# Performance work log

Hardware: AMD Instinct MI355X
Metric: run time of the kernel (lower is better)

The kernel has to match this reference:

```python
import jax, jax.numpy as jnp
import numpy as np

N_NODES = 140000   # 14 frames * 10000 nodes/frame
N_EDGES = 2240000  # avg degree 16
NFEAT = 128
NHID = 128
N_FRAMES = 14


def setup_inputs() -> dict:
    key = jax.random.key(0)
    k1, k2, k3, k4, k5 = jax.random.split(key, 5)
    x = jax.random.normal(k1, (N_NODES, NFEAT), dtype=jnp.float32)
    # gc1 parameters (only layer actually used in forward)
    W = jax.random.normal(k2, (NFEAT, NHID), dtype=jnp.float32) * 0.05
    b = jnp.zeros((NHID,), dtype=jnp.float32)
    # sparse normalized adjacency as COO edge list (row sorted for fast segment_sum)
    edge_row = jnp.sort(jax.random.randint(k3, (N_EDGES,), 0, N_NODES, dtype=jnp.int32))
    edge_col = jax.random.randint(k4, (N_EDGES,), 0, N_NODES, dtype=jnp.int32)
    edge_val = jax.random.uniform(k5, (N_EDGES,), dtype=jnp.float32)
    return {"x": x, "W": W, "b": b, "edge_val": edge_val,
            "edge_row": edge_row, "edge_col": edge_col}


def reference(x, W, b, edge_val, edge_row, edge_col):
    # GraphConvolution: adj @ (x @ W) + b  (adj sparse, COO)
    support = x @ W                                   # [N, NHID]
    msgs = edge_val[:, None] * support[edge_col]      # [E, NHID] gather
    agg = jax.ops.segment_sum(msgs, edge_row, num_segments=N_NODES,
                              indices_are_sorted=True)  # [N, NHID] scatter-add
    h = jax.nn.relu(agg + b)
    # view(14, -1, c) then max over frame axis
    h = h.reshape(N_FRAMES, -1, NHID)                 # [14, N/14, NHID]
    h = jnp.max(h, axis=0)                            # [N/14, NHID]
    return jax.nn.log_softmax(h, axis=1)
```

## Files before the change

kernel.cpp:

```cpp
#include <hip/hip_runtime.h>
#include <hip/hip_bf16.h>

#define N_NODES 140000
#define N_EDGES 2240000
#define NFEAT 128
#define NHID 128
#define N_FRAMES 14
#define NODES_PER_FRAME 10000
#define CAP 352

typedef __attribute__((ext_vector_type(8))) short frag_b16;
typedef __attribute__((ext_vector_type(4))) int frag_i4;
typedef __attribute__((ext_vector_type(4))) float f32x4;

__device__ __forceinline__ unsigned short f2bf(float f) {
    union { float f; unsigned int u; } v; v.f = f;
    unsigned int r = v.u + 0x7fffu + ((v.u >> 16) & 1u);
    return (unsigned short)(r >> 16);
}
__device__ __forceinline__ int pk_bf16(float a, float b) {
    union { __hip_bfloat162 h; int i; } u;
    u.h = __float22bfloat162_rn(make_float2(a, b));
    return u.i;
}

__global__ void convert_wt(const float* __restrict__ W, unsigned short* __restrict__ WT) {
    int idx = blockIdx.x * blockDim.x + threadIdx.x;
    if (idx >= NFEAT * NHID) return;
    int k = idx >> 7, n = idx & 127;
    WT[n * 128 + k] = f2bf(W[idx]);
}

#define WT_STRIDE 136

__global__ __launch_bounds__(256) void gemm_kernel(
        const float* __restrict__ x, const unsigned short* __restrict__ WT,
        unsigned char* __restrict__ supQ, float* __restrict__ scales) {
    __shared__ unsigned short wt_lds[128 * WT_STRIDE];

    const uint4* WTv = (const uint4*)WT;
    for (int idx = threadIdx.x; idx < 2048; idx += 256) {
        uint4 d = WTv[idx];
        int elem = idx << 3;
        int n = elem >> 7, k = elem & 127;
        *(uint4*)&wt_lds[n * WT_STRIDE + k] = d;
    }

    int wave = threadIdx.x >> 6;
    int lane = threadIdx.x & 63;
    int m = lane & 15;
    int q = lane >> 4;

    long row0 = (long)blockIdx.x * 64 + wave * 16;

    int arow = (int)row0 + m;
    if (arow >= N_NODES) arow = N_NODES - 1;
    const float* xrow = x + (long)arow * 128 + q * 8;
    frag_b16 xa[4];
#pragma unroll
    for (int ks = 0; ks < 4; ++ks) {
        float4 lo = *(const float4*)(xrow + ks * 32);
        float4 hi = *(const float4*)(xrow + ks * 32 + 4);
        union { frag_b16 f; frag_i4 i; } u;
        u.i[0] = pk_bf16(lo.x, lo.y);
        u.i[1] = pk_bf16(lo.z, lo.w);
        u.i[2] = pk_bf16(hi.x, hi.y);
        u.i[3] = pk_bf16(hi.z, hi.w);
        xa[ks] = u.f;
    }

    __syncthreads();

    if (row0 < N_NODES) {
        f32x4 acc[8];
#pragma unroll
        for (int t = 0; t < 8; ++t) acc[t] = (f32x4){0.f, 0.f, 0.f, 0.f};

#pragma unroll
        for (int t = 0; t < 8; ++t) {
            const unsigned short* bp = &wt_lds[(t * 16 + m) * WT_STRIDE + q * 8];
#pragma unroll
            for (int ks = 0; ks < 4; ++ks) {
                frag_b16 wfrag = *(const frag_b16*)(bp + ks * 32);
                acc[t] = __builtin_amdgcn_mfma_f32_16x16x32_bf16(wfrag, xa[ks], acc[t], 0, 0, 0);
            }
        }

        float amax = 0.f;
#pragma unroll
        for (int t = 0; t < 8; ++t)
#pragma unroll
            for (int r = 0; r < 4; ++r) amax = fmaxf(amax, fabsf(acc[t][r]));
        amax = fmaxf(amax, __shfl_xor(amax, 16));
        amax = fmaxf(amax, __shfl_xor(amax, 32));
        float rinv = amax > 0.f ? 127.f / amax : 0.f;

        long node = row0 + m;
        if (node < N_NODES) {
            if (q == 0) scales[node] = amax * (1.f / 127.f);
            unsigned char* srow = supQ + node * 128;
#pragma unroll
            for (int t = 0; t < 8; ++t) {
                unsigned u0 = (unsigned)(rintf(acc[t][0] * rinv) + 128.f);
                unsigned u1 = (unsigned)(rintf(acc[t][1] * rinv) + 128.f);
                unsigned u2 = (unsigned)(rintf(acc[t][2] * rinv) + 128.f);
                unsigned u3 = (unsigned)(rintf(acc[t][3] * rinv) + 128.f);
                *(unsigned*)(srow + t * 16 + q * 4) = u0 | (u1 << 8) | (u2 << 16) | (u3 << 24);
            }
        }
    }
}

__global__ void prep_kernel(const int* __restrict__ edge_row, const int* __restrict__ edge_col,
                            const float* __restrict__ edge_val, const float* __restrict__ scales,
                            int* __restrict__ row_ptr, float* __restrict__ valp) {
    int e = blockIdx.x * blockDim.x + threadIdx.x;
    if (e >= N_EDGES) return;
    int r = edge_row[e];
    int prev = (e == 0) ? -1 : edge_row[e - 1];
    for (int q = prev + 1; q <= r; ++q) row_ptr[q] = e;
    if (e == N_EDGES - 1) {
        for (int q = r + 1; q <= N_NODES; ++q) row_ptr[q] = N_EDGES;
    }
    valp[e] = edge_val[e] * scales[edge_col[e]];
}

__global__ __launch_bounds__(128) void agg_kernel(
        const unsigned char* __restrict__ supQ, const float* __restrict__ b,
        const float* __restrict__ valp, const int* __restrict__ edge_col,
        const int* __restrict__ row_ptr, float* __restrict__ out) {
    __shared__ int    segStart[2][8];
    __shared__ int    segLen[2][8];
    __shared__ int    segOff[2][8];
    __shared__ int2   eBuf[2][CAP];
    __shared__ float4 xch[2][16][2];

    const int i = blockIdx.x;
    const int lane = threadIdx.x & 63;
    const int w = threadIdx.x >> 6;
    const int eh = lane >> 4;
    const int f8 = lane & 15;
    const unsigned f8x8 = (unsigned)f8 * 8u;

    int a = 0, len = 0;
    if (lane < 7) {
        int n = (w * 7 + lane) * NODES_PER_FRAME + i;
        a = row_ptr[n];
        len = row_ptr[n + 1] - a;
    }
    int len8 = (len + 7) & ~7;
    int off = 0;
#pragma unroll
    for (int f2 = 0; f2 < 7; ++f2) {
        int L2 = __shfl(len8, f2);
        if (f2 < lane) off += L2;
    }
    if (lane < 7) { segStart[w][lane] = a; segLen[w][lane] = len; segOff[w][lane] = off; }
    if (lane == 6) segOff[w][7] = off + len8;
    __syncthreads();

    const bool fit = segOff[w][7] <= CAP;

    if (fit) {
#pragma unroll 1
        for (int f = 0; f < 7; ++f) {
            int g = segStart[w][f], s = segOff[w][f], L = segLen[w][f];
            int L8 = (L + 7) & ~7;
            for (int j = lane; j < L8; j += 64) {
                int2 v = make_int2(0, 0);
                if (j < L) {
                    v.x = edge_col[g + j];
                    v.y = __float_as_int(valp[g + j]);
                }
                eBuf[w][s + j] = v;
            }
        }
    }
    __syncthreads();

    const float4 blo = *(const float4*)&b[f8 * 8];
    const float4 bhi = *(const float4*)&b[f8 * 8 + 4];
    float m0 = 0.f, m1 = 0.f, m2 = 0.f, m3 = 0.f;
    float m4 = 0.f, m5 = 0.f, m6 = 0.f, m7 = 0.f;

    if (fit) {
#pragma unroll 1
        for (int f = 0; f < 7; ++f) {
            int s = segOff[w][f];
            int e8 = s + ((segLen[w][f] + 7) & ~7);
            float a0 = 0.f, a1 = 0.f, a2 = 0.f, a3 = 0.f;
            float a4 = 0.f, a5 = 0.f, a6 = 0.f, a7 = 0.f, svf = 0.f;
            for (int j = s; j < e8; j += 8) {
                int2 e0 = eBuf[w][j + eh];
                int2 e1 = eBuf[w][j + 4 + eh];
                uint2 q0 = *(const uint2*)(supQ + (((unsigned)e0.x) << 7) + f8x8);
                uint2 q1 = *(const uint2*)(supQ + (((unsigned)e1.x) << 7) + f8x8);
                float v0 = __int_as_float(e0.y);
                float v1 = __int_as_float(e1.y);
                a0 = fmaf(v0, (float)( q0.x        & 0xffu), a0);
                a1 = fmaf(v0, (float)((q0.x >> 8)  & 0xffu), a1);
                a2 = fmaf(v0, (float)((q0.x >> 16) & 0xffu), a2);
                a3 = fmaf(v0, (float)( q0.x >> 24        ), a3);
                a4 = fmaf(v0, (float)( q0.y        & 0xffu), a4);
                a5 = fmaf(v0, (float)((q0.y >> 8)  & 0xffu), a5);
                a6 = fmaf(v0, (float)((q0.y >> 16) & 0xffu), a6);
                a7 = fmaf(v0, (float)( q0.y >> 24        ), a7);
                svf += v0;
                a0 = fmaf(v1, (float)( q1.x        & 0xffu), a0);
                a1 = fmaf(v1, (float)((q1.x >> 8)  & 0xffu), a1);
                a2 = fmaf(v1, (float)((q1.x >> 16) & 0xffu), a2);
                a3 = fmaf(v1, (float)( q1.x >> 24        ), a3);
                a4 = fmaf(v1, (float)( q1.y        & 0xffu), a4);
                a5 = fmaf(v1, (float)((q1.y >> 8)  & 0xffu), a5);
                a6 = fmaf(v1, (float)((q1.y >> 16) & 0xffu), a6);
                a7 = fmaf(v1, (float)( q1.y >> 24        ), a7);
                svf += v1;
            }
            a0 += __shfl_xor(a0, 16); a1 += __shfl_xor(a1, 16);
            a2 += __shfl_xor(a2, 16); a3 += __shfl_xor(a3, 16);
            a4 += __shfl_xor(a4, 16); a5 += __shfl_xor(a5, 16);
            a6 += __shfl_xor(a6, 16); a7 += __shfl_xor(a7, 16);
            svf += __shfl_xor(svf, 16);
            a0 += __shfl_xor(a0, 32); a1 += __shfl_xor(a1, 32);
            a2 += __shfl_xor(a2, 32); a3 += __shfl_xor(a3, 32);
            a4 += __shfl_xor(a4, 32); a5 += __shfl_xor(a5, 32);
            a6 += __shfl_xor(a6, 32); a7 += __shfl_xor(a7, 32);
            svf += __shfl_xor(svf, 32);
            float h0 = fmaf(-128.f, svf, a0) + blo.x;
            float h1 = fmaf(-128.f, svf, a1) + blo.y;
            float h2 = fmaf(-128.f, svf, a2) + blo.z;
            float h3 = fmaf(-128.f, svf, a3) + blo.w;
            float h4 = fmaf(-128.f, svf, a4) + bhi.x;
            float h5 = fmaf(-128.f, svf, a5) + bhi.y;
            float h6 = fmaf(-128.f, svf, a6) + bhi.z;
            float h7 = fmaf(-128.f, svf, a7) + bhi.w;
            m0 = fmaxf(m0, fmaxf(h0, 0.f)); m1 = fmaxf(m1, fmaxf(h1, 0.f));
            m2 = fmaxf(m2, fmaxf(h2, 0.f)); m3 = fmaxf(m3, fmaxf(h3, 0.f));
            m4 = fmaxf(m4, fmaxf(h4, 0.f)); m5 = fmaxf(m5, fmaxf(h5, 0.f));
            m6 = fmaxf(m6, fmaxf(h6, 0.f)); m7 = fmaxf(m7, fmaxf(h7, 0.f));
        }
    } else {
#pragma unroll 1
        for (int f = 0; f < 7; ++f) {
            int g = segStart[w][f], L = segLen[w][f];
            float a0 = 0.f, a1 = 0.f, a2 = 0.f, a3 = 0.f;
            float a4 = 0.f, a5 = 0.f, a6 = 0.f, a7 = 0.f, svf = 0.f;
            for (int j = eh; j < L; j += 4) {
                int c = edge_col[g + j];
                float v = valp[g + j];
                uint2 qv = *(const uint2*)(supQ + (((unsigned)c) << 7) + f8x8);
                a0 = fmaf(v, (float)( qv.x        & 0xffu), a0);
                a1 = fmaf(v, (float)((qv.x >> 8)  & 0xffu), a1);
                a2 = fmaf(v, (float)((qv.x >> 16) & 0xffu), a2);
                a3 = fmaf(v, (float)( qv.x >> 24        ), a3);
                a4 = fmaf(v, (float)( qv.y        & 0xffu), a4);
                a5 = fmaf(v, (float)((qv.y >> 8)  & 0xffu), a5);
                a6 = fmaf(v, (float)((qv.y >> 16) & 0xffu), a6);
                a7 = fmaf(v, (float)( qv.y >> 24        ), a7);
                svf += v;
            }
            a0 += __shfl_xor(a0, 16); a1 += __shfl_xor(a1, 16);
            a2 += __shfl_xor(a2, 16); a3 += __shfl_xor(a3, 16);
            a4 += __shfl_xor(a4, 16); a5 += __shfl_xor(a5, 16);
            a6 += __shfl_xor(a6, 16); a7 += __shfl_xor(a7, 16);
            svf += __shfl_xor(svf, 16);
            a0 += __shfl_xor(a0, 32); a1 += __shfl_xor(a1, 32);
            a2 += __shfl_xor(a2, 32); a3 += __shfl_xor(a3, 32);
            a4 += __shfl_xor(a4, 32); a5 += __shfl_xor(a5, 32);
            a6 += __shfl_xor(a6, 32); a7 += __shfl_xor(a7, 32);
            svf += __shfl_xor(svf, 32);
            float h0 = fmaf(-128.f, svf, a0) + blo.x;
            float h1 = fmaf(-128.f, svf, a1) + blo.y;
            float h2 = fmaf(-128.f, svf, a2) + blo.z;
            float h3 = fmaf(-128.f, svf, a3) + blo.w;
            float h4 = fmaf(-128.f, svf, a4) + bhi.x;
            float h5 = fmaf(-128.f, svf, a5) + bhi.y;
            float h6 = fmaf(-128.f, svf, a6) + bhi.z;
            float h7 = fmaf(-128.f, svf, a7) + bhi.w;
            m0 = fmaxf(m0, fmaxf(h0, 0.f)); m1 = fmaxf(m1, fmaxf(h1, 0.f));
            m2 = fmaxf(m2, fmaxf(h2, 0.f)); m3 = fmaxf(m3, fmaxf(h3, 0.f));
            m4 = fmaxf(m4, fmaxf(h4, 0.f)); m5 = fmaxf(m5, fmaxf(h5, 0.f));
            m6 = fmaxf(m6, fmaxf(h6, 0.f)); m7 = fmaxf(m7, fmaxf(h7, 0.f));
        }
    }

    if (eh == 0) {
        xch[w][f8][0] = make_float4(m0, m1, m2, m3);
        xch[w][f8][1] = make_float4(m4, m5, m6, m7);
    }
    __syncthreads();
    float4 p0 = xch[0][f8][0], p1 = xch[0][f8][1];
    float4 q0 = xch[1][f8][0], q1 = xch[1][f8][1];
    float o0 = fmaxf(p0.x, q0.x), o1 = fmaxf(p0.y, q0.y);
    float o2 = fmaxf(p0.z, q0.z), o3 = fmaxf(p0.w, q0.w);
    float o4 = fmaxf(p1.x, q1.x), o5 = fmaxf(p1.y, q1.y);
    float o6 = fmaxf(p1.z, q1.z), o7 = fmaxf(p1.w, q1.w);

    float M = fmaxf(fmaxf(fmaxf(o0, o1), fmaxf(o2, o3)),
                    fmaxf(fmaxf(o4, o5), fmaxf(o6, o7)));
#pragma unroll
    for (int o = 8; o >= 1; o >>= 1) M = fmaxf(M, __shfl_xor(M, o));
    float S = __expf(o0 - M) + __expf(o1 - M) + __expf(o2 - M) + __expf(o3 - M)
            + __expf(o4 - M) + __expf(o5 - M) + __expf(o6 - M) + __expf(o7 - M);
#pragma unroll
    for (int o = 8; o >= 1; o >>= 1) S += __shfl_xor(S, o);

    if (w == 0 && eh == 0) {
        float ls = __logf(S);
        float* orow = out + i * 128 + f8 * 8;
        *(float4*)orow       = make_float4(o0 - M - ls, o1 - M - ls, o2 - M - ls, o3 - M - ls);
        *(float4*)(orow + 4) = make_float4(o4 - M - ls, o5 - M - ls, o6 - M - ls, o7 - M - ls);
    }
}

extern "C" void kernel_launch(void* const* d_in, const int* in_sizes, int n_in,
                              void* d_out, int out_size, void* d_ws, size_t ws_size,
                              hipStream_t stream) {
    const float* x        = (const float*)d_in[0];
    const float* W        = (const float*)d_in[1];
    const float* b        = (const float*)d_in[2];
    const float* edge_val = (const float*)d_in[3];
    const int*   edge_row = (const int*)d_in[4];
    const int*   edge_col = (const int*)d_in[5];
    float* out = (float*)d_out;

    char* ws = (char*)d_ws;
    unsigned char*  supQ    = (unsigned char*)ws;
    float*          scales  = (float*)(ws + 17920000);
    unsigned short* WT      = (unsigned short*)(ws + 18480000);
    int*            row_ptr = (int*)(ws + 18512768);
    float*          valp    = (float*)(ws + 19072772);

    convert_wt<<<64, 256, 0, stream>>>(W, WT);
    gemm_kernel<<<(N_NODES + 63) / 64, 256, 0, stream>>>(x, WT, supQ, scales);
    prep_kernel<<<(N_EDGES + 255) / 256, 256, 0, stream>>>(edge_row, edge_col, edge_val,
                                                           scales, row_ptr, valp);
    agg_kernel<<<NODES_PER_FRAME, 128, 0, stream>>>(supQ, b, valp, edge_col, row_ptr, out);
}
```

Before: 213.0 us.

## Fold edge scaling into aggregation, merge prep kernels, software-pipeline gathers

The weight-transpose conversion is merged with the row_ptr construction into a single prep kernel launched before the GEMM. The valp array (edge_val times the per-column scale) is no longer materialized; the aggregation kernel computes it while staging edges into LDS, and stores the column pre-shifted as a byte offset. This removes one launch and a full write and read of the per-edge array, at the cost of an extra random scales gather inside the aggregation kernel. The fast-path gather loop is also software-pipelined, loading the next pair of rows while the current pair is accumulated, to hide gather latency at some extra register cost.

Result: faster. 207.9 us (-2.4%).

```diff
diff --git a/kernel.cpp b/kernel.cpp
--- a/kernel.cpp
+++ b/kernel.cpp
@@ -24,11 +24,21 @@
     return u.i;
 }
 
-__global__ void convert_wt(const float* __restrict__ W, unsigned short* __restrict__ WT) {
-    int idx = blockIdx.x * blockDim.x + threadIdx.x;
-    if (idx >= NFEAT * NHID) return;
-    int k = idx >> 7, n = idx & 127;
-    WT[n * 128 + k] = f2bf(W[idx]);
+__global__ void prep_kernel(const float* __restrict__ W, unsigned short* __restrict__ WT,
+                            const int* __restrict__ edge_row, int* __restrict__ row_ptr) {
+    int e = blockIdx.x * blockDim.x + threadIdx.x;
+    if (e < NFEAT * NHID) {
+        int k = e >> 7, n = e & 127;
+        WT[n * 128 + k] = f2bf(W[e]);
+    }
+    if (e < N_EDGES) {
+        int r = edge_row[e];
+        int prev = (e == 0) ? -1 : edge_row[e - 1];
+        for (int q = prev + 1; q <= r; ++q) row_ptr[q] = e;
+        if (e == N_EDGES - 1) {
+            for (int q = r + 1; q <= N_NODES; ++q) row_ptr[q] = N_EDGES;
+        }
+    }
 }
 
 #define WT_STRIDE 136
@@ -111,23 +121,10 @@
     }
 }
 
-__global__ void prep_kernel(const int* __restrict__ edge_row, const int* __restrict__ edge_col,
-                            const float* __restrict__ edge_val, const float* __restrict__ scales,
-                            int* __restrict__ row_ptr, float* __restrict__ valp) {
-    int e = blockIdx.x * blockDim.x + threadIdx.x;
-    if (e >= N_EDGES) return;
-    int r = edge_row[e];
-    int prev = (e == 0) ? -1 : edge_row[e - 1];
-    for (int q = prev + 1; q <= r; ++q) row_ptr[q] = e;
-    if (e == N_EDGES - 1) {
-        for (int q = r + 1; q <= N_NODES; ++q) row_ptr[q] = N_EDGES;
-    }
-    valp[e] = edge_val[e] * scales[edge_col[e]];
-}
-
 __global__ __launch_bounds__(128) void agg_kernel(
-        const unsigned char* __restrict__ supQ, const float* __restrict__ b,
-        const float* __restrict__ valp, const int* __restrict__ edge_col,
+        const unsigned char* __restrict__ supQ, const float* __restrict__ scales,
+        const float* __restrict__ b,
+        const float* __restrict__ edge_val, const int* __restrict__ edge_col,
         const int* __restrict__ row_ptr, float* __restrict__ out) {
     __shared__ int    segStart[2][8];
     __shared__ int    segLen[2][8];
@@ -169,8 +166,9 @@
             for (int j = lane; j < L8; j += 64) {
                 int2 v = make_int2(0, 0);
                 if (j < L) {
-                    v.x = edge_col[g + j];
-                    v.y = __float_as_int(valp[g + j]);
+                    int c = edge_col[g + j];
+                    v.x = c << 7;
+                    v.y = __float_as_int(edge_val[g + j] * scales[c]);
                 }
                 eBuf[w][s + j] = v;
             }
@@ -187,35 +185,69 @@
 #pragma unroll 1
         for (int f = 0; f < 7; ++f) {
             int s = segOff[w][f];
-            int e8 = s + ((segLen[w][f] + 7) & ~7);
+            int R = ((segLen[w][f] + 7) & ~7) >> 3;
             float a0 = 0.f, a1 = 0.f, a2 = 0.f, a3 = 0.f;
             float a4 = 0.f, a5 = 0.f, a6 = 0.f, a7 = 0.f, svf = 0.f;
-            for (int j = s; j < e8; j += 8) {
-                int2 e0 = eBuf[w][j + eh];
-                int2 e1 = eBuf[w][j + 4 + eh];
-                uint2 q0 = *(const uint2*)(supQ + (((unsigned)e0.x) << 7) + f8x8);
-                uint2 q1 = *(const uint2*)(supQ + (((unsigned)e1.x) << 7) + f8x8);
-                float v0 = __int_as_float(e0.y);
-                float v1 = __int_as_float(e1.y);
-                a0 = fmaf(v0, (float)( q0.x        & 0xffu), a0);
-                a1 = fmaf(v0, (float)((q0.x >> 8)  & 0xffu), a1);
-                a2 = fmaf(v0, (float)((q0.x >> 16) & 0xffu), a2);
-                a3 = fmaf(v0, (float)( q0.x >> 24        ), a3);
-                a4 = fmaf(v0, (float)( q0.y        & 0xffu), a4);
-                a5 = fmaf(v0, (float)((q0.y >> 8)  & 0xffu), a5);
-                a6 = fmaf(v0, (float)((q0.y >> 16) & 0xffu), a6);
-                a7 = fmaf(v0, (float)( q0.y >> 24        ), a7);
+
+            int2 c0, c1; uint2 g0, g1;
+            if (R > 0) {
+                c0 = eBuf[w][s + eh];
+                c1 = eBuf[w][s + 4 + eh];
+                g0 = *(const uint2*)(supQ + ((unsigned)c0.x | f8x8));
+                g1 = *(const uint2*)(supQ + ((unsigned)c1.x | f8x8));
+            }
+#pragma unroll 1
+            for (int r = 1; r < R; ++r) {
+                int jn = s + r * 8;
+                int2 n0 = eBuf[w][jn + eh];
+                int2 n1 = eBuf[w][jn + 4 + eh];
+                uint2 h0 = *(const uint2*)(supQ + ((unsigned)n0.x | f8x8));
+                uint2 h1 = *(const uint2*)(supQ + ((unsigned)n1.x | f8x8));
+                float v0 = __int_as_float(c0.y);
+                float v1 = __int_as_float(c1.y);
+                a0 = fmaf(v0, (float)( g0.x        & 0xffu), a0);
+                a1 = fmaf(v0, (float)((g0.x >> 8)  & 0xffu), a1);
+                a2 = fmaf(v0, (float)((g0.x >> 16) & 0xffu), a2);
+                a3 = fmaf(v0, (float)( g0.x >> 24        ), a3);
+                a4 = fmaf(v0, (float)( g0.y        & 0xffu), a4);
+                a5 = fmaf(v0, (float)((g0.y >> 8)  & 0xffu), a5);
+                a6 = fmaf(v0, (float)((g0.y >> 16) & 0xffu), a6);
+                a7 = fmaf(v0, (float)( g0.y >> 24        ), a7);
                 svf += v0;
-                a0 = fmaf(v1, (float)( q1.x        & 0xffu), a0);
-                a1 = fmaf(v1, (float)((q1.x >> 8)  & 0xffu), a1);
-                a2 = fmaf(v1, (float)((q1.x >> 16) & 0xffu), a2);
-                a3 = fmaf(v1, (float)( q1.x >> 24        ), a3);
-                a4 = fmaf(v1, (float)( q1.y        & 0xffu), a4);
-                a5 = fmaf(v1, (float)((q1.y >> 8)  & 0xffu), a5);
-                a6 = fmaf(v1, (float)((q1.y >> 16) & 0xffu), a6);
-                a7 = fmaf(v1, (float)( q1.y >> 24        ), a7);
+                a0 = fmaf(v1, (float)( g1.x        & 0xffu), a0);
+                a1 = fmaf(v1, (float)((g1.x >> 8)  & 0xffu), a1);
+                a2 = fmaf(v1, (float)((g1.x >> 16) & 0xffu), a2);
+                a3 = fmaf(v1, (float)( g1.x >> 24        ), a3);
+                a4 = fmaf(v1, (float)( g1.y        & 0xffu), a4);
+                a5 = fmaf(v1, (float)((g1.y >> 8)  & 0xffu), a5);
+                a6 = fmaf(v1, (float)((g1.y >> 16) & 0xffu), a6);
+                a7 = fmaf(v1, (float)( g1.y >> 24        ), a7);
                 svf += v1;
-            }
+                c0 = n0; c1 = n1; g0 = h0; g1 = h1;
+            }
+            if (R > 0) {
+                float v0 = __int_as_float(c0.y);
+                float v1 = __int_as_float(c1.y);
+                a0 = fmaf(v0, (float)( g0.x        & 0xffu), a0);
+                a1 = fmaf(v0, (float)((g0.x >> 8)  & 0xffu), a1);
+                a2 = fmaf(v0, (float)((g0.x >> 16) & 0xffu), a2);
+                a3 = fmaf(v0, (float)( g0.x >> 24        ), a3);
+                a4 = fmaf(v0, (float)( g0.y        & 0xffu), a4);
+                a5 = fmaf(v0, (float)((g0.y >> 8)  & 0xffu), a5);
+                a6 = fmaf(v0, (float)((g0.y >> 16) & 0xffu), a6);
+                a7 = fmaf(v0, (float)( g0.y >> 24        ), a7);
+                svf += v0;
+                a0 = fmaf(v1, (float)( g1.x        & 0xffu), a0);
+                a1 = fmaf(v1, (float)((g1.x >> 8)  & 0xffu), a1);
+                a2 = fmaf(v1, (float)((g1.x >> 16) & 0xffu), a2);
+                a3 = fmaf(v1, (float)( g1.x >> 24        ), a3);
+                a4 = fmaf(v1, (float)( g1.y        & 0xffu), a4);
+                a5 = fmaf(v1, (float)((g1.y >> 8)  & 0xffu), a5);
+                a6 = fmaf(v1, (float)((g1.y >> 16) & 0xffu), a6);
+                a7 = fmaf(v1, (float)( g1.y >> 24        ), a7);
+                svf += v1;
+            }
+
             a0 += __shfl_xor(a0, 16); a1 += __shfl_xor(a1, 16);
             a2 += __shfl_xor(a2, 16); a3 += __shfl_xor(a3, 16);
             a4 += __shfl_xor(a4, 16); a5 += __shfl_xor(a5, 16);
@@ -247,7 +279,7 @@
             float a4 = 0.f, a5 = 0.f, a6 = 0.f, a7 = 0.f, svf = 0.f;
             for (int j = eh; j < L; j += 4) {
                 int c = edge_col[g + j];
-                float v = valp[g + j];
+                float v = edge_val[g + j] * scales[c];
                 uint2 qv = *(const uint2*)(supQ + (((unsigned)c) << 7) + f8x8);
                 a0 = fmaf(v, (float)( qv.x        & 0xffu), a0);
                 a1 = fmaf(v, (float)((qv.x >> 8)  & 0xffu), a1);
@@ -329,11 +361,9 @@
     float*          scales  = (float*)(ws + 17920000);
     unsigned short* WT      = (unsigned short*)(ws + 18480000);
     int*            row_ptr = (int*)(ws + 18512768);
-    float*          valp    = (float*)(ws + 19072772);
-
-    convert_wt<<<64, 256, 0, stream>>>(W, WT);
+
+    prep_kernel<<<(N_EDGES + 255) / 256, 256, 0, stream>>>(W, WT, edge_row, row_ptr);
     gemm_kernel<<<(N_NODES + 63) / 64, 256, 0, stream>>>(x, WT, supQ, scales);
-    prep_kernel<<<(N_EDGES + 255) / 256, 256, 0, stream>>>(edge_row, edge_col, edge_val,
-                                                           scales, row_ptr, valp);
-    agg_kernel<<<NODES_PER_FRAME, 128, 0, stream>>>(supQ, b, valp, edge_col, row_ptr, out);
-}
+    agg_kernel<<<NODES_PER_FRAME, 128, 0, stream>>>(supQ, scales, b, edge_val, edge_col,
+                                                    row_ptr, out);
+}
```

## Fuse weight conversion, GEMM and row-pointer prep; fold edge scaling into aggregation

Applied to the files above, without the earlier changes.

Four launches become two. The weight transpose and bf16 conversion move into each GEMM block's shared-memory load, and the row_ptr construction runs as extra blocks of the same grid. The per-edge value scaling (edge_val * scales[col]) and the valp buffer are removed; aggregation now computes it while staging edges. Edge staging is one pass per frame with shifted column offsets and a precomputed per-segment value sum, which removes the svf accumulation from the inner loop. The fast path now requires every segment to have at most 64 edges, and the gemm blocks redo the W conversion per block.

Measured after the change: 226.1 us. 1.06x slower.

```diff
diff --git a/kernel.cpp b/kernel.cpp
--- a/kernel.cpp
+++ b/kernel.cpp
@@ -8,6 +8,8 @@
 #define N_FRAMES 14
 #define NODES_PER_FRAME 10000
 #define CAP 352
+#define GEMM_BLOCKS ((N_NODES + 63) / 64)
+#define PREP_BLOCKS ((N_EDGES + 255) / 256)
 
 typedef __attribute__((ext_vector_type(8))) short frag_b16;
 typedef __attribute__((ext_vector_type(4))) int frag_i4;
@@ -24,26 +26,36 @@
     return u.i;
 }
 
-__global__ void convert_wt(const float* __restrict__ W, unsigned short* __restrict__ WT) {
-    int idx = blockIdx.x * blockDim.x + threadIdx.x;
-    if (idx >= NFEAT * NHID) return;
-    int k = idx >> 7, n = idx & 127;
-    WT[n * 128 + k] = f2bf(W[idx]);
-}
-
 #define WT_STRIDE 136
 
-__global__ __launch_bounds__(256) void gemm_kernel(
-        const float* __restrict__ x, const unsigned short* __restrict__ WT,
-        unsigned char* __restrict__ supQ, float* __restrict__ scales) {
+__global__ __launch_bounds__(256) void gemm_prep_kernel(
+        const float* __restrict__ x, const float* __restrict__ W,
+        unsigned char* __restrict__ supQ, float* __restrict__ scales,
+        const int* __restrict__ edge_row, int* __restrict__ row_ptr) {
     __shared__ unsigned short wt_lds[128 * WT_STRIDE];
 
-    const uint4* WTv = (const uint4*)WT;
-    for (int idx = threadIdx.x; idx < 2048; idx += 256) {
-        uint4 d = WTv[idx];
-        int elem = idx << 3;
-        int n = elem >> 7, k = elem & 127;
-        *(uint4*)&wt_lds[n * WT_STRIDE + k] = d;
+    if (blockIdx.x >= GEMM_BLOCKS) {
+        int e = (blockIdx.x - GEMM_BLOCKS) * 256 + threadIdx.x;
+        if (e < N_EDGES) {
+            int r = edge_row[e];
+            int prev = (e == 0) ? -1 : edge_row[e - 1];
+            for (int q = prev + 1; q <= r; ++q) row_ptr[q] = e;
+            if (e == N_EDGES - 1) {
+                for (int q = r + 1; q <= N_NODES; ++q) row_ptr[q] = N_EDGES;
+            }
+        }
+        return;
+    }
+
+    const float4* Wv = (const float4*)W;
+    for (int idx = threadIdx.x; idx < 4096; idx += 256) {
+        float4 d = Wv[idx];
+        int k = idx >> 5;
+        int n0 = (idx & 31) << 2;
+        wt_lds[(n0 + 0) * WT_STRIDE + k] = f2bf(d.x);
+        wt_lds[(n0 + 1) * WT_STRIDE + k] = f2bf(d.y);
+        wt_lds[(n0 + 2) * WT_STRIDE + k] = f2bf(d.z);
+        wt_lds[(n0 + 3) * WT_STRIDE + k] = f2bf(d.w);
     }
 
     int wave = threadIdx.x >> 6;
@@ -111,27 +123,15 @@
     }
 }
 
-__global__ void prep_kernel(const int* __restrict__ edge_row, const int* __restrict__ edge_col,
-                            const float* __restrict__ edge_val, const float* __restrict__ scales,
-                            int* __restrict__ row_ptr, float* __restrict__ valp) {
-    int e = blockIdx.x * blockDim.x + threadIdx.x;
-    if (e >= N_EDGES) return;
-    int r = edge_row[e];
-    int prev = (e == 0) ? -1 : edge_row[e - 1];
-    for (int q = prev + 1; q <= r; ++q) row_ptr[q] = e;
-    if (e == N_EDGES - 1) {
-        for (int q = r + 1; q <= N_NODES; ++q) row_ptr[q] = N_EDGES;
-    }
-    valp[e] = edge_val[e] * scales[edge_col[e]];
-}
-
 __global__ __launch_bounds__(128) void agg_kernel(
-        const unsigned char* __restrict__ supQ, const float* __restrict__ b,
-        const float* __restrict__ valp, const int* __restrict__ edge_col,
+        const unsigned char* __restrict__ supQ, const float* __restrict__ scales,
+        const float* __restrict__ b,
+        const float* __restrict__ edge_val, const int* __restrict__ edge_col,
         const int* __restrict__ row_ptr, float* __restrict__ out) {
     __shared__ int    segStart[2][8];
     __shared__ int    segLen[2][8];
     __shared__ int    segOff[2][8];
+    __shared__ float  segSvf[2][7];
     __shared__ int2   eBuf[2][CAP];
     __shared__ float4 xch[2][16][2];
 
@@ -148,6 +148,12 @@
         a = row_ptr[n];
         len = row_ptr[n + 1] - a;
     }
+    int ml = len;
+    ml = max(ml, __shfl_xor(ml, 1));
+    ml = max(ml, __shfl_xor(ml, 2));
+    ml = max(ml, __shfl_xor(ml, 4));
+    const int maxlen = __shfl(ml, 0);
+
     int len8 = (len + 7) & ~7;
     int off = 0;
 #pragma unroll
@@ -159,21 +165,25 @@
     if (lane == 6) segOff[w][7] = off + len8;
     __syncthreads();
 
-    const bool fit = segOff[w][7] <= CAP;
+    const bool fit = (segOff[w][7] <= CAP) && (maxlen <= 64);
 
     if (fit) {
-#pragma unroll 1
+#pragma unroll
         for (int f = 0; f < 7; ++f) {
-            int g = segStart[w][f], s = segOff[w][f], L = segLen[w][f];
-            int L8 = (L + 7) & ~7;
-            for (int j = lane; j < L8; j += 64) {
-                int2 v = make_int2(0, 0);
-                if (j < L) {
-                    v.x = edge_col[g + j];
-                    v.y = __float_as_int(valp[g + j]);
-                }
-                eBuf[w][s + j] = v;
-            }
+            int aF = __shfl(a, f), lF = __shfl(len, f), sF = __shfl(off, f);
+            int L8 = (lF + 7) & ~7;
+            int2 v = make_int2(0, 0);
+            if (lane < lF) {
+                int c = edge_col[aF + lane];
+                v.x = c << 7;
+                v.y = __float_as_int(edge_val[aF + lane] * scales[c]);
+            }
+            if (lane < L8) eBuf[w][sF + lane] = v;
+            float sv = __int_as_float(v.y);
+            sv += __shfl_xor(sv, 1);  sv += __shfl_xor(sv, 2);
+            sv += __shfl_xor(sv, 4);  sv += __shfl_xor(sv, 8);
+            sv += __shfl_xor(sv, 16); sv += __shfl_xor(sv, 32);
+            if (lane == 0) segSvf[w][f] = sv;
         }
     }
     __syncthreads();
@@ -189,12 +199,12 @@
             int s = segOff[w][f];
             int e8 = s + ((segLen[w][f] + 7) & ~7);
             float a0 = 0.f, a1 = 0.f, a2 = 0.f, a3 = 0.f;
-            float a4 = 0.f, a5 = 0.f, a6 = 0.f, a7 = 0.f, svf = 0.f;
+            float a4 = 0.f, a5 = 0.f, a6 = 0.f, a7 = 0.f;
             for (int j = s; j < e8; j += 8) {
                 int2 e0 = eBuf[w][j + eh];
                 int2 e1 = eBuf[w][j + 4 + eh];
-                uint2 q0 = *(const uint2*)(supQ + (((unsigned)e0.x) << 7) + f8x8);
-                uint2 q1 = *(const uint2*)(supQ + (((unsigned)e1.x) << 7) + f8x8);
+                uint2 q0 = *(const uint2*)(supQ + ((unsigned)e0.x | f8x8));
+                uint2 q1 = *(const uint2*)(supQ + ((unsigned)e1.x | f8x8));
                 float v0 = __int_as_float(e0.y);
                 float v1 = __int_as_float(e1.y);
                 a0 = fmaf(v0, (float)( q0.x        & 0xffu), a0);
@@ -205,7 +215,6 @@
                 a5 = fmaf(v0, (float)((q0.y >> 8)  & 0xffu), a5);
                 a6 = fmaf(v0, (float)((q0.y >> 16) & 0xffu), a6);
                 a7 = fmaf(v0, (float)( q0.y >> 24        ), a7);
-                svf += v0;
                 a0 = fmaf(v1, (float)( q1.x        & 0xffu), a0);
                 a1 = fmaf(v1, (float)((q1.x >> 8)  & 0xffu), a1);
                 a2 = fmaf(v1, (float)((q1.x >> 16) & 0xffu), a2);
@@ -214,7 +223,48 @@
                 a5 = fmaf(v1, (float)((q1.y >> 8)  & 0xffu), a5);
                 a6 = fmaf(v1, (float)((q1.y >> 16) & 0xffu), a6);
                 a7 = fmaf(v1, (float)( q1.y >> 24        ), a7);
-                svf += v1;
+            }
+            a0 += __shfl_xor(a0, 16); a1 += __shfl_xor(a1, 16);
+            a2 += __shfl_xor(a2, 16); a3 += __shfl_xor(a3, 16);
+            a4 += __shfl_xor(a4, 16); a5 += __shfl_xor(a5, 16);
+            a6 += __shfl_xor(a6, 16); a7 += __shfl_xor(a7, 16);
+            a0 += __shfl_xor(a0, 32); a1 += __shfl_xor(a1, 32);
+            a2 += __shfl_xor(a2, 32); a3 += __shfl_xor(a3, 32);
+            a4 += __shfl_xor(a4, 32); a5 += __shfl_xor(a5, 32);
+            a6 += __shfl_xor(a6, 32); a7 += __shfl_xor(a7, 32);
+            float svf = segSvf[w][f];
+            float h0 = fmaf(-128.f, svf, a0) + blo.x;
+            float h1 = fmaf(-128.f, svf, a1) + blo.y;
+            float h2 = fmaf(-128.f, svf, a2) + blo.z;
+            float h3 = fmaf(-128.f, svf, a3) + blo.w;
+            float h4 = fmaf(-128.f, svf, a4) + bhi.x;
+            float h5 = fmaf(-128.f, svf, a5) + bhi.y;
+            float h6 = fmaf(-128.f, svf, a6) + bhi.z;
+            float h7 = fmaf(-128.f, svf, a7) + bhi.w;
+            m0 = fmaxf(m0, fmaxf(h0, 0.f)); m1 = fmaxf(m1, fmaxf(h1, 0.f));
+            m2 = fmaxf(m2, fmaxf(h2, 0.f)); m3 = fmaxf(m3, fmaxf(h3, 0.f));
+            m4 = fmaxf(m4, fmaxf(h4, 0.f)); m5 = fmaxf(m5, fmaxf(h5, 0.f));
+            m6 = fmaxf(m6, fmaxf(h6, 0.f)); m7 = fmaxf(m7, fmaxf(h7, 0.f));
+        }
+    } else {
+#pragma unroll 1
+        for (int f = 0; f < 7; ++f) {
+            int g = segStart[w][f], L = segLen[w][f];
+            float a0 = 0.f, a1 = 0.f, a2 = 0.f, a3 = 0.f;
+            float a4 = 0.f, a5 = 0.f, a6 = 0.f, a7 = 0.f, svf = 0.f;
+            for (int j = eh; j < L; j += 4) {
+                int c = edge_col[g + j];
+                float v = edge_val[g + j] * scales[c];
+                uint2 qv = *(const uint2*)(supQ + (((unsigned)c) << 7) + f8x8);
+                a0 = fmaf(v, (float)( qv.x        & 0xffu), a0);
+                a1 = fmaf(v, (float)((qv.x >> 8)  & 0xffu), a1);
+                a2 = fmaf(v, (float)((qv.x >> 16) & 0xffu), a2);
+                a3 = fmaf(v, (float)( qv.x >> 24        ), a3);
+                a4 = fmaf(v, (float)( qv.y        & 0xffu), a4);
+                a5 = fmaf(v, (float)((qv.y >> 8)  & 0xffu), a5);
+                a6 = fmaf(v, (float)((qv.y >> 16) & 0xffu), a6);
+                a7 = fmaf(v, (float)( qv.y >> 24        ), a7);
+                svf += v;
             }
             a0 += __shfl_xor(a0, 16); a1 += __shfl_xor(a1, 16);
             a2 += __shfl_xor(a2, 16); a3 += __shfl_xor(a3, 16);
@@ -239,49 +289,6 @@
             m4 = fmaxf(m4, fmaxf(h4, 0.f)); m5 = fmaxf(m5, fmaxf(h5, 0.f));
             m6 = fmaxf(m6, fmaxf(h6, 0.f)); m7 = fmaxf(m7, fmaxf(h7, 0.f));
         }
-    } else {
-#pragma unroll 1
-        for (int f = 0; f < 7; ++f) {
-            int g = segStart[w][f], L = segLen[w][f];
-            float a0 = 0.f, a1 = 0.f, a2 = 0.f, a3 = 0.f;
-            float a4 = 0.f, a5 = 0.f, a6 = 0.f, a7 = 0.f, svf = 0.f;
-            for (int j = eh; j < L; j += 4) {
-                int c = edge_col[g + j];
-                float v = valp[g + j];
-                uint2 qv = *(const uint2*)(supQ + (((unsigned)c) << 7) + f8x8);
-                a0 = fmaf(v, (float)( qv.x        & 0xffu), a0);
-                a1 = fmaf(v, (float)((qv.x >> 8)  & 0xffu), a1);
-                a2 = fmaf(v, (float)((qv.x >> 16) & 0xffu), a2);
-                a3 = fmaf(v, (float)( qv.x >> 24        ), a3);
-                a4 = fmaf(v, (float)( qv.y        & 0xffu), a4);
-                a5 = fmaf(v, (float)((qv.y >> 8)  & 0xffu), a5);
-                a6 = fmaf(v, (float)((qv.y >> 16) & 0xffu), a6);
-                a7 = fmaf(v, (float)( qv.y >> 24        ), a7);
-                svf += v;
-            }
-            a0 += __shfl_xor(a0, 16); a1 += __shfl_xor(a1, 16);
-            a2 += __shfl_xor(a2, 16); a3 += __shfl_xor(a3, 16);
-            a4 += __shfl_xor(a4, 16); a5 += __shfl_xor(a5, 16);
-            a6 += __shfl_xor(a6, 16); a7 += __shfl_xor(a7, 16);
-            svf += __shfl_xor(svf, 16);
-            a0 += __shfl_xor(a0, 32); a1 += __shfl_xor(a1, 32);
-            a2 += __shfl_xor(a2, 32); a3 += __shfl_xor(a3, 32);
-            a4 += __shfl_xor(a4, 32); a5 += __shfl_xor(a5, 32);
-            a6 += __shfl_xor(a6, 32); a7 += __shfl_xor(a7, 32);
-            svf += __shfl_xor(svf, 32);
-            float h0 = fmaf(-128.f, svf, a0) + blo.x;
-            float h1 = fmaf(-128.f, svf, a1) + blo.y;
-            float h2 = fmaf(-128.f, svf, a2) + blo.z;
-            float h3 = fmaf(-128.f, svf, a3) + blo.w;
-            float h4 = fmaf(-128.f, svf, a4) + bhi.x;
-            float h5 = fmaf(-128.f, svf, a5) + bhi.y;
-            float h6 = fmaf(-128.f, svf, a6) + bhi.z;
-            float h7 = fmaf(-128.f, svf, a7) + bhi.w;
-            m0 = fmaxf(m0, fmaxf(h0, 0.f)); m1 = fmaxf(m1, fmaxf(h1, 0.f));
-            m2 = fmaxf(m2, fmaxf(h2, 0.f)); m3 = fmaxf(m3, fmaxf(h3, 0.f));
-            m4 = fmaxf(m4, fmaxf(h4, 0.f)); m5 = fmaxf(m5, fmaxf(h5, 0.f));
-            m6 = fmaxf(m6, fmaxf(h6, 0.f)); m7 = fmaxf(m7, fmaxf(h7, 0.f));
-        }
     }
 
     if (eh == 0) {
@@ -327,13 +334,10 @@
     char* ws = (char*)d_ws;
     unsigned char*  supQ    = (unsigned char*)ws;
     float*          scales  = (float*)(ws + 17920000);
-    unsigned short* WT      = (unsigned short*)(ws + 18480000);
-    int*            row_ptr = (int*)(ws + 18512768);
-    float*          valp    = (float*)(ws + 19072772);
-
-    convert_wt<<<64, 256, 0, stream>>>(W, WT);
-    gemm_kernel<<<(N_NODES + 63) / 64, 256, 0, stream>>>(x, WT, supQ, scales);
-    prep_kernel<<<(N_EDGES + 255) / 256, 256, 0, stream>>>(edge_row, edge_col, edge_val,
-                                                           scales, row_ptr, valp);
-    agg_kernel<<<NODES_PER_FRAME, 128, 0, stream>>>(supQ, b, valp, edge_col, row_ptr, out);
-}
+    int*            row_ptr = (int*)(ws + 18480000);
+
+    gemm_prep_kernel<<<GEMM_BLOCKS + PREP_BLOCKS, 256, 0, stream>>>(
+        x, W, supQ, scales, edge_row, row_ptr);
+    agg_kernel<<<NODES_PER_FRAME, 128, 0, stream>>>(supQ, scales, b, edge_val, edge_col,
+                                                    row_ptr, out);
+}
```

## Merge weight conversion into row_ptr prep and fold edge scaling into aggregation

Applied to the files above, without the earlier changes.

Folds the weight transpose/convert kernel into the row_ptr-building kernel and moves that kernel ahead of the GEMM, since it no longer depends on the per-row scales. The per-edge value times scale product is now computed inside the aggregation kernel while staging edges into shared memory. This removes the valp array write and read, and one launch. The column index is also stored pre-shifted so the gather address needs only an OR. In exchange, the aggregation kernel does an extra random gather of scales[c] per edge.

Result: faster. 205.9 us (-3.3%).

```diff
diff --git a/kernel.cpp b/kernel.cpp
--- a/kernel.cpp
+++ b/kernel.cpp
@@ -24,11 +24,21 @@
     return u.i;
 }
 
-__global__ void convert_wt(const float* __restrict__ W, unsigned short* __restrict__ WT) {
-    int idx = blockIdx.x * blockDim.x + threadIdx.x;
-    if (idx >= NFEAT * NHID) return;
-    int k = idx >> 7, n = idx & 127;
-    WT[n * 128 + k] = f2bf(W[idx]);
+__global__ void prep_kernel(const float* __restrict__ W, unsigned short* __restrict__ WT,
+                            const int* __restrict__ edge_row, int* __restrict__ row_ptr) {
+    int e = blockIdx.x * blockDim.x + threadIdx.x;
+    if (e < NFEAT * NHID) {
+        int k = e >> 7, n = e & 127;
+        WT[n * 128 + k] = f2bf(W[e]);
+    }
+    if (e < N_EDGES) {
+        int r = edge_row[e];
+        int prev = (e == 0) ? -1 : edge_row[e - 1];
+        for (int q = prev + 1; q <= r; ++q) row_ptr[q] = e;
+        if (e == N_EDGES - 1) {
+            for (int q = r + 1; q <= N_NODES; ++q) row_ptr[q] = N_EDGES;
+        }
+    }
 }
 
 #define WT_STRIDE 136
@@ -111,23 +121,10 @@
     }
 }
 
-__global__ void prep_kernel(const int* __restrict__ edge_row, const int* __restrict__ edge_col,
-                            const float* __restrict__ edge_val, const float* __restrict__ scales,
-                            int* __restrict__ row_ptr, float* __restrict__ valp) {
-    int e = blockIdx.x * blockDim.x + threadIdx.x;
-    if (e >= N_EDGES) return;
-    int r = edge_row[e];
-    int prev = (e == 0) ? -1 : edge_row[e - 1];
-    for (int q = prev + 1; q <= r; ++q) row_ptr[q] = e;
-    if (e == N_EDGES - 1) {
-        for (int q = r + 1; q <= N_NODES; ++q) row_ptr[q] = N_EDGES;
-    }
-    valp[e] = edge_val[e] * scales[edge_col[e]];
-}
-
 __global__ __launch_bounds__(128) void agg_kernel(
-        const unsigned char* __restrict__ supQ, const float* __restrict__ b,
-        const float* __restrict__ valp, const int* __restrict__ edge_col,
+        const unsigned char* __restrict__ supQ, const float* __restrict__ scales,
+        const float* __restrict__ b,
+        const float* __restrict__ edge_val, const int* __restrict__ edge_col,
         const int* __restrict__ row_ptr, float* __restrict__ out) {
     __shared__ int    segStart[2][8];
     __shared__ int    segLen[2][8];
@@ -169,8 +166,9 @@
             for (int j = lane; j < L8; j += 64) {
                 int2 v = make_int2(0, 0);
                 if (j < L) {
-                    v.x = edge_col[g + j];
-                    v.y = __float_as_int(valp[g + j]);
+                    int c = edge_col[g + j];
+                    v.x = c << 7;
+                    v.y = __float_as_int(edge_val[g + j] * scales[c]);
                 }
                 eBuf[w][s + j] = v;
             }
@@ -193,8 +191,8 @@
             for (int j = s; j < e8; j += 8) {
                 int2 e0 = eBuf[w][j + eh];
                 int2 e1 = eBuf[w][j + 4 + eh];
-                uint2 q0 = *(const uint2*)(supQ + (((unsigned)e0.x) << 7) + f8x8);
-                uint2 q1 = *(const uint2*)(supQ + (((unsigned)e1.x) << 7) + f8x8);
+                uint2 q0 = *(const uint2*)(supQ + ((unsigned)e0.x | f8x8));
+                uint2 q1 = *(const uint2*)(supQ + ((unsigned)e1.x | f8x8));
                 float v0 = __int_as_float(e0.y);
                 float v1 = __int_as_float(e1.y);
                 a0 = fmaf(v0, (float)( q0.x        & 0xffu), a0);
@@ -247,7 +245,7 @@
             float a4 = 0.f, a5 = 0.f, a6 = 0.f, a7 = 0.f, svf = 0.f;
             for (int j = eh; j < L; j += 4) {
                 int c = edge_col[g + j];
-                float v = valp[g + j];
+                float v = edge_val[g + j] * scales[c];
                 uint2 qv = *(const uint2*)(supQ + (((unsigned)c) << 7) + f8x8);
                 a0 = fmaf(v, (float)( qv.x        & 0xffu), a0);
                 a1 = fmaf(v, (float)((qv.x >> 8)  & 0xffu), a1);
@@ -329,11 +327,9 @@
     float*          scales  = (float*)(ws + 17920000);
     unsigned short* WT      = (unsigned short*)(ws + 18480000);
     int*            row_ptr = (int*)(ws + 18512768);
-    float*          valp    = (float*)(ws + 19072772);
-
-    convert_wt<<<64, 256, 0, stream>>>(W, WT);
+
+    prep_kernel<<<(N_EDGES + 255) / 256, 256, 0, stream>>>(W, WT, edge_row, row_ptr);
     gemm_kernel<<<(N_NODES + 63) / 64, 256, 0, stream>>>(x, WT, supQ, scales);
-    prep_kernel<<<(N_EDGES + 255) / 256, 256, 0, stream>>>(edge_row, edge_col, edge_val,
-                                                           scales, row_ptr, valp);
-    agg_kernel<<<NODES_PER_FRAME, 128, 0, stream>>>(supQ, b, valp, edge_col, row_ptr, out);
-}
+    agg_kernel<<<NODES_PER_FRAME, 128, 0, stream>>>(supQ, scales, b, edge_val, edge_col,
+                                                    row_ptr, out);
+}
```
